# Optimization experiments

Measured on AMD Instinct MI355X. Metric: run time of the kernel, lower is better.

## Reference

```python
import jax, jax.numpy as jnp
import numpy as np

EPS = 1e-7


def setup_inputs() -> dict:
    key = jax.random.key(0)
    k1, k2 = jax.random.split(key)
    N, C = 16384, 10000
    pred = jax.random.normal(k1, (N, C), dtype=jnp.float32)
    labels = jax.random.randint(k2, (N,), 0, C)
    return {"pred": pred, "labels": labels}


def reference(pred, labels):
    N, C = pred.shape
    # randomness of the torch module (random negative offsets + np.random.rand gate),
    # made deterministic/on-device with a fixed key
    k_off, k_u = jax.random.split(jax.random.key(42))
    offsets = jax.random.randint(k_off, (N,), 1, C)          # random_(1, C)
    rand_u = jax.random.uniform(k_u, (N,), dtype=jnp.float32)  # np.random.rand per sample

    target_neg = (labels + offsets) % C                       # shifted-label negatives

    norms = jnp.linalg.norm(pred, axis=-1, keepdims=True) + EPS  # [N,1]
    logit_norm = pred / norms / 2.0
    snorm = jax.nn.softmax(logit_norm, axis=1) + EPS          # [N,C]
    log_snorm = jnp.log(snorm)

    max_prob = jnp.max(snorm, axis=1)                         # argmax_snorm[0]
    argmax = jnp.argmax(snorm, axis=1)                        # argmax_snorm[1]
    # vectorized form of the per-sample loop: replace negative with argmax class
    replace = (rand_u <= max_prob) & (argmax != labels)
    target_neg = jnp.where(replace, argmax, target_neg)

    rows = jnp.arange(N)
    # (1 - onehot(labels)) * log_snorm summed == full row sum minus label entry
    pos_term = (log_snorm.sum(axis=1) - log_snorm[rows, labels]).mean()
    neg_term = log_snorm[rows, target_neg].mean()
    loss = 10.0 * (pos_term - neg_term)
    return (loss, jnp.squeeze(norms))
```

## Files before the change

kernel.cpp:

```cpp
#include <hip/hip_runtime.h>
#include <stdint.h>

#define NROWS 16384
#define NC    10000
#define NF4   2500
#define BLK   256
#define WPB   4
#define NBLK  (NROWS / WPB)
#define EPSF  1e-7f

struct U2 { uint32_t a, b; };

__host__ __device__ constexpr U2 tf2x32(uint32_t k0, uint32_t k1,
                                        uint32_t x0, uint32_t x1) {
  const uint32_t ks2 = k0 ^ k1 ^ 0x1BD11BDAu;
  uint32_t v0 = x0 + k0, v1 = x1 + k1;
#define TF_R(r) { v0 += v1; v1 = (v1 << (r)) | (v1 >> (32 - (r))); v1 ^= v0; }
  TF_R(13) TF_R(15) TF_R(26) TF_R(6)
  v0 += k1;  v1 += ks2 + 1u;
  TF_R(17) TF_R(29) TF_R(16) TF_R(24)
  v0 += ks2; v1 += k0 + 2u;
  TF_R(13) TF_R(15) TF_R(26) TF_R(6)
  v0 += k0;  v1 += k1 + 3u;
  TF_R(17) TF_R(29) TF_R(16) TF_R(24)
  v0 += k1;  v1 += ks2 + 4u;
  TF_R(13) TF_R(15) TF_R(26) TF_R(6)
  v0 += ks2; v1 += k0 + 5u;
#undef TF_R
  return {v0, v1};
}

constexpr U2 KA = tf2x32(0u, 42u, 0u, 0u);
constexpr U2 KB = tf2x32(0u, 42u, 0u, 1u);

__global__ __launch_bounds__(BLK, 8)
void nnce_rows(const float* __restrict__ pred,
               const int* __restrict__ labels,
               float* __restrict__ out,
               float* __restrict__ row_acc)
{
  const int tid  = threadIdx.x;
  const int lane = tid & 63;
  const int wid  = tid >> 6;
  const int row  = blockIdx.x * WPB + wid;
  const float*  p  = pred + (size_t)row * NC;
  const float4* p4 = (const float4*)p;

  const int lab = labels[row];
  const uint32_t xin = (uint32_t)row + ((lane == 1) ? (uint32_t)NROWS : 0u);
  const uint32_t kk0 = (lane == 2) ? KB.a : KA.a;
  const uint32_t kk1 = (lane == 2) ? KB.b : KA.b;
  const U2 rr = tf2x32(kk0, kk1, 0u, xin);
  const uint32_t hb  = __shfl((int)rr.b, 0, 64);
  const uint32_t lob = __shfl((int)rr.b, 1, 64);
  const uint32_t ub  = __shfl((int)rr.b, 2, 64);
  const uint32_t span = 9999u, mult = 6835u;
  const uint32_t off = ((hb % span) * mult + (lob % span)) % span;
  const float ru = __uint_as_float((ub >> 9) | 0x3F800000u) - 1.0f;
  const int cand1 = (lab + 1 + (int)off) % NC;
  const float p_lab = p[lab];
  const float p_c1  = p[cand1];

  float sp = 0.f, ss = 0.f, sc = 0.f, sq = 0.f, mv = -1e30f;
  int mi = 0;

#define PROC1(xv, e) { const float q_ = (xv) * (xv);            \
    sp += (xv); ss += q_;                                        \
    sc = fmaf(q_, (xv), sc); sq = fmaf(q_, q_, sq);              \
    if ((xv) > mv) { mv = (xv); mi = (e); } }
#define PROC4(v, e) { PROC1((v).x, (e)); PROC1((v).y, (e) + 1);  \
                      PROC1((v).z, (e) + 2); PROC1((v).w, (e) + 3); }

  int k = lane;
#pragma unroll 1
  for (int it = 0; it < 9; ++it) {
    const float4 a = p4[k], b = p4[k + 64], c = p4[k + 128], d = p4[k + 192];
    PROC4(a, 4 * k);
    PROC4(b, 4 * (k + 64));
    PROC4(c, 4 * (k + 128));
    PROC4(d, 4 * (k + 192));
    k += 256;
  }
  {
    const float4 a = p4[k], b = p4[k + 64], c = p4[k + 128];
    PROC4(a, 4 * k);
    PROC4(b, 4 * (k + 64));
    PROC4(c, 4 * (k + 128));
  }
  if (lane < 4) {
    const float4 t = p4[2496 + lane];
    PROC4(t, 4 * (2496 + lane));
  }
#undef PROC4
#undef PROC1

  for (int o = 32; o > 0; o >>= 1) {
    sp += __shfl_xor(sp, o, 64);
    ss += __shfl_xor(ss, o, 64);
    sc += __shfl_xor(sc, o, 64);
    sq += __shfl_xor(sq, o, 64);
    const float om = __shfl_xor(mv, o, 64);
    const int   oi = __shfl_xor(mi, o, 64);
    if (om > mv || (om == mv && oi < mi)) { mv = om; mi = oi; }
  }

  const float norm  = sqrtf(ss) + EPSF;
  const float inv2n = 0.5f / norm;
  const float i2    = inv2n * inv2n;
  const float t1 = sp * inv2n;
  const float t2 = 0.5f * ss * i2;
  const float t3 = (1.0f / 6.0f) * sc * i2 * inv2n;
  const float t4 = (1.0f / 24.0f) * sq * i2 * i2;
  const float Z    = (float)NC + t1 + t2 + t3 + t4;
  const float Zm   = (float)NC - t1 + t2 - t3 + t4;
  const float logZ = logf(Z);
  const float eZ   = EPSF * Z;

  const float max_prob = __expf(mv * inv2n) / Z + EPSF;
  const bool  replace  = (ru <= max_prob) && (mi != lab);
  const float p_neg    = replace ? mv : p_c1;

  const float x_lab  = p_lab * inv2n;
  const float x_neg  = p_neg * inv2n;
  const float ls_lab = x_lab + eZ * (1.0f - x_lab) - logZ;
  const float ls_neg = x_neg + eZ * (1.0f - x_neg) - logZ;
  const float sumlog = t1 + eZ * Zm - (float)NC * logZ;

  if (lane == 0) {
    out[1 + row]  = norm;
    row_acc[row]  = (sumlog - ls_lab) - ls_neg;
  }
}

__global__ __launch_bounds__(1024)
void nnce_final(const float* __restrict__ row_acc, float* __restrict__ out) {
  __shared__ double red[1024];
  double s = 0.0;
  for (int i = threadIdx.x; i < NROWS; i += 1024) s += (double)row_acc[i];
  red[threadIdx.x] = s;
  __syncthreads();
  for (int k = 512; k > 0; k >>= 1) {
    if (threadIdx.x < k) red[threadIdx.x] += red[threadIdx.x + k];
    __syncthreads();
  }
  if (threadIdx.x == 0) out[0] = (float)(10.0 * red[0] / (double)NROWS);
}

extern "C" void kernel_launch(void* const* d_in, const int* in_sizes, int n_in,
                              void* d_out, int out_size, void* d_ws, size_t ws_size,
                              hipStream_t stream) {
  const float* pred   = (const float*)d_in[0];
  const int*   labels = (const int*)d_in[1];
  float* out     = (float*)d_out;
  float* row_acc = (float*)d_ws;

  nnce_rows<<<NBLK, BLK, 0, stream>>>(pred, labels, out, row_acc);
  nnce_final<<<1, 1024, 0, stream>>>(row_acc, out);
}
```

Measured before the change: 125.9 us.

## Fuse final reduction via fixed-point atomics and drop argmax index tracking

Replaces the second reduction kernel with per-block fixed-point 64-bit atomic adds into 256 cells, where the last block to finish (found through a counter atomic) sums the cells and writes the loss. It also stops tracking the argmax index: only the max value is kept, and the replace test compares the max against the label's value instead of comparing indices. The aim is to save the second kernel launch and cut per-element compare and select work in the streaming loop. In exchange it adds a memset, atomics, and a last-block pattern, and it can differ from the reference when the max ties with the label's value or a fixed-point value rounds.

```diff
diff --git a/kernel.cpp b/kernel.cpp
--- a/kernel.cpp
+++ b/kernel.cpp
@@ -7,7 +7,9 @@
 #define BLK   256
 #define WPB   4
 #define NBLK  (NROWS / WPB)
+#define NCELL 256
 #define EPSF  1e-7f
+#define SCALE 262144.0
 
 struct U2 { uint32_t a, b; };
 
@@ -37,8 +39,11 @@
 void nnce_rows(const float* __restrict__ pred,
                const int* __restrict__ labels,
                float* __restrict__ out,
-               float* __restrict__ row_acc)
+               unsigned long long* __restrict__ ws)
 {
+  __shared__ long long lred[WPB];
+  __shared__ int lflag;
+
   const int tid  = threadIdx.x;
   const int lane = tid & 63;
   const int wid  = tid >> 6;
@@ -62,34 +67,27 @@
   const float p_c1  = p[cand1];
 
   float sp = 0.f, ss = 0.f, sc = 0.f, sq = 0.f, mv = -1e30f;
-  int mi = 0;
 
-#define PROC1(xv, e) { const float q_ = (xv) * (xv);            \
+#define PROC1(xv) { const float q_ = (xv) * (xv);               \
     sp += (xv); ss += q_;                                        \
     sc = fmaf(q_, (xv), sc); sq = fmaf(q_, q_, sq);              \
-    if ((xv) > mv) { mv = (xv); mi = (e); } }
-#define PROC4(v, e) { PROC1((v).x, (e)); PROC1((v).y, (e) + 1);  \
-                      PROC1((v).z, (e) + 2); PROC1((v).w, (e) + 3); }
+    mv = fmaxf(mv, (xv)); }
+#define PROC4(v) { PROC1((v).x); PROC1((v).y); PROC1((v).z); PROC1((v).w); }
 
   int k = lane;
 #pragma unroll 1
   for (int it = 0; it < 9; ++it) {
     const float4 a = p4[k], b = p4[k + 64], c = p4[k + 128], d = p4[k + 192];
-    PROC4(a, 4 * k);
-    PROC4(b, 4 * (k + 64));
-    PROC4(c, 4 * (k + 128));
-    PROC4(d, 4 * (k + 192));
+    PROC4(a); PROC4(b); PROC4(c); PROC4(d);
     k += 256;
   }
   {
     const float4 a = p4[k], b = p4[k + 64], c = p4[k + 128];
-    PROC4(a, 4 * k);
-    PROC4(b, 4 * (k + 64));
-    PROC4(c, 4 * (k + 128));
+    PROC4(a); PROC4(b); PROC4(c);
   }
   if (lane < 4) {
     const float4 t = p4[2496 + lane];
-    PROC4(t, 4 * (2496 + lane));
+    PROC4(t);
   }
 #undef PROC4
 #undef PROC1
@@ -99,9 +97,7 @@
     ss += __shfl_xor(ss, o, 64);
     sc += __shfl_xor(sc, o, 64);
     sq += __shfl_xor(sq, o, 64);
-    const float om = __shfl_xor(mv, o, 64);
-    const int   oi = __shfl_xor(mi, o, 64);
-    if (om > mv || (om == mv && oi < mi)) { mv = om; mi = oi; }
+    mv  = fmaxf(mv, __shfl_xor(mv, o, 64));
   }
 
   const float norm  = sqrtf(ss) + EPSF;
@@ -117,7 +113,7 @@
   const float eZ   = EPSF * Z;
 
   const float max_prob = __expf(mv * inv2n) / Z + EPSF;
-  const bool  replace  = (ru <= max_prob) && (mi != lab);
+  const bool  replace  = (ru <= max_prob) && (mv != p_lab);
   const float p_neg    = replace ? mv : p_c1;
 
   const float x_lab  = p_lab * inv2n;
@@ -126,24 +122,33 @@
   const float ls_neg = x_neg + eZ * (1.0f - x_neg) - logZ;
   const float sumlog = t1 + eZ * Zm - (float)NC * logZ;
 
+  const float val = (sumlog - ls_lab) - ls_neg;
+
   if (lane == 0) {
-    out[1 + row]  = norm;
-    row_acc[row]  = (sumlog - ls_lab) - ls_neg;
+    out[1 + row] = norm;
+    const long long fx = (long long)((double)val * SCALE);
+    atomicAdd(&ws[1 + (blockIdx.x & (NCELL - 1))], (unsigned long long)fx);
   }
-}
 
-__global__ __launch_bounds__(1024)
-void nnce_final(const float* __restrict__ row_acc, float* __restrict__ out) {
-  __shared__ double red[1024];
-  double s = 0.0;
-  for (int i = threadIdx.x; i < NROWS; i += 1024) s += (double)row_acc[i];
-  red[threadIdx.x] = s;
   __syncthreads();
-  for (int k = 512; k > 0; k >>= 1) {
-    if (threadIdx.x < k) red[threadIdx.x] += red[threadIdx.x + k];
+  if (tid == 0) {
+    __threadfence();
+    const unsigned long long old = atomicAdd(&ws[0], 1ULL);
+    lflag = (old == (unsigned long long)(NBLK - 1)) ? 1 : 0;
+  }
+  __syncthreads();
+  if (lflag) {
+    long long v = 0;
+    if (tid < NCELL) v = (long long)atomicAdd(&ws[1 + tid], 0ULL);
+    for (int o = 32; o > 0; o >>= 1) v += __shfl_down(v, o, 64);
+    if (lane == 0) lred[wid] = v;
     __syncthreads();
+    if (tid == 0) {
+      long long t = 0;
+      for (int w = 0; w < WPB; ++w) t += lred[w];
+      out[0] = (float)(10.0 * ((double)t / SCALE) / (double)NROWS);
+    }
   }
-  if (threadIdx.x == 0) out[0] = (float)(10.0 * red[0] / (double)NROWS);
 }
 
 extern "C" void kernel_launch(void* const* d_in, const int* in_sizes, int n_in,
@@ -151,9 +156,9 @@
                               hipStream_t stream) {
   const float* pred   = (const float*)d_in[0];
   const int*   labels = (const int*)d_in[1];
-  float* out     = (float*)d_out;
-  float* row_acc = (float*)d_ws;
+  float* out = (float*)d_out;
+  unsigned long long* ws = (unsigned long long*)d_ws;
 
-  nnce_rows<<<NBLK, BLK, 0, stream>>>(pred, labels, out, row_acc);
-  nnce_final<<<1, 1024, 0, stream>>>(row_acc, out);
+  hipMemsetAsync(d_ws, 0, (1 + NCELL) * sizeof(unsigned long long), stream);
+  nnce_rows<<<NBLK, BLK, 0, stream>>>(pred, labels, out, ws);
 }
```

Result: slower. 320.1 us (+154.3%).

## Prefetch next row chunk, drop argmax index tracking, shrink blocks, shuffle-reduce final

Applied to the files above, without the earlier changes.

The row kernel now loads the next four float4 chunks while it processes the current ones, a software-pipelined loop. It also replaces argmax index tracking with a plain fmaxf max, comparing the max value to the label's value instead of comparing indices. Blocks shrink from 4 to 2 waves. The final reduction uses float4 loads and wave shuffles instead of a shared-memory tree. The value comparison can decide differently from the index comparison when the label's value ties the row max, and the prefetch raises register pressure.

```diff
diff --git a/kernel.cpp b/kernel.cpp
--- a/kernel.cpp
+++ b/kernel.cpp
@@ -4,8 +4,8 @@
 #define NROWS 16384
 #define NC    10000
 #define NF4   2500
-#define BLK   256
-#define WPB   4
+#define BLK   128
+#define WPB   2
 #define NBLK  (NROWS / WPB)
 #define EPSF  1e-7f
 
@@ -62,35 +62,30 @@
   const float p_c1  = p[cand1];
 
   float sp = 0.f, ss = 0.f, sc = 0.f, sq = 0.f, mv = -1e30f;
-  int mi = 0;
 
-#define PROC1(xv, e) { const float q_ = (xv) * (xv);            \
+#define PROC1(xv) { const float q_ = (xv) * (xv);               \
     sp += (xv); ss += q_;                                        \
     sc = fmaf(q_, (xv), sc); sq = fmaf(q_, q_, sq);              \
-    if ((xv) > mv) { mv = (xv); mi = (e); } }
-#define PROC4(v, e) { PROC1((v).x, (e)); PROC1((v).y, (e) + 1);  \
-                      PROC1((v).z, (e) + 2); PROC1((v).w, (e) + 3); }
+    mv = fmaxf(mv, (xv)); }
+#define PROC4(v) { PROC1((v).x); PROC1((v).y); PROC1((v).z); PROC1((v).w); }
 
   int k = lane;
+  float4 c0 = p4[k], c1 = p4[k + 64], c2 = p4[k + 128], c3 = p4[k + 192];
 #pragma unroll 1
-  for (int it = 0; it < 9; ++it) {
-    const float4 a = p4[k], b = p4[k + 64], c = p4[k + 128], d = p4[k + 192];
-    PROC4(a, 4 * k);
-    PROC4(b, 4 * (k + 64));
-    PROC4(c, 4 * (k + 128));
-    PROC4(d, 4 * (k + 192));
+  for (int it = 0; it < 8; ++it) {
+    const float4 n0 = p4[k + 256], n1 = p4[k + 320],
+                 n2 = p4[k + 384], n3 = p4[k + 448];
+    PROC4(c0); PROC4(c1); PROC4(c2); PROC4(c3);
+    c0 = n0; c1 = n1; c2 = n2; c3 = n3;
     k += 256;
   }
-  {
-    const float4 a = p4[k], b = p4[k + 64], c = p4[k + 128];
-    PROC4(a, 4 * k);
-    PROC4(b, 4 * (k + 64));
-    PROC4(c, 4 * (k + 128));
-  }
-  if (lane < 4) {
-    const float4 t = p4[2496 + lane];
-    PROC4(t, 4 * (2496 + lane));
-  }
+  const float4 e0 = p4[k + 256], e1 = p4[k + 320], e2 = p4[k + 384];
+  float4 tl;
+  const bool hast = (lane < 4);
+  if (hast) tl = p4[2496 + lane];
+  PROC4(c0); PROC4(c1); PROC4(c2); PROC4(c3);
+  PROC4(e0); PROC4(e1); PROC4(e2);
+  if (hast) PROC4(tl);
 #undef PROC4
 #undef PROC1
 
@@ -99,9 +94,7 @@
     ss += __shfl_xor(ss, o, 64);
     sc += __shfl_xor(sc, o, 64);
     sq += __shfl_xor(sq, o, 64);
-    const float om = __shfl_xor(mv, o, 64);
-    const int   oi = __shfl_xor(mi, o, 64);
-    if (om > mv || (om == mv && oi < mi)) { mv = om; mi = oi; }
+    mv  = fmaxf(mv, __shfl_xor(mv, o, 64));
   }
 
   const float norm  = sqrtf(ss) + EPSF;
@@ -117,7 +110,7 @@
   const float eZ   = EPSF * Z;
 
   const float max_prob = __expf(mv * inv2n) / Z + EPSF;
-  const bool  replace  = (ru <= max_prob) && (mi != lab);
+  const bool  replace  = (ru <= max_prob) && (mv != p_lab);
   const float p_neg    = replace ? mv : p_c1;
 
   const float x_lab  = p_lab * inv2n;
@@ -127,23 +120,31 @@
   const float sumlog = t1 + eZ * Zm - (float)NC * logZ;
 
   if (lane == 0) {
-    out[1 + row]  = norm;
-    row_acc[row]  = (sumlog - ls_lab) - ls_neg;
+    out[1 + row] = norm;
+    row_acc[row] = (sumlog - ls_lab) - ls_neg;
   }
 }
 
-__global__ __launch_bounds__(1024)
+__global__ __launch_bounds__(512)
 void nnce_final(const float* __restrict__ row_acc, float* __restrict__ out) {
-  __shared__ double red[1024];
+  __shared__ double lred[8];
+  const int tid  = threadIdx.x;
+  const int lane = tid & 63;
+  const int wid  = tid >> 6;
+  const float4* r4 = (const float4*)row_acc;
   double s = 0.0;
-  for (int i = threadIdx.x; i < NROWS; i += 1024) s += (double)row_acc[i];
-  red[threadIdx.x] = s;
+  for (int i = tid; i < NROWS / 4; i += 512) {
+    const float4 v = r4[i];
+    s += (double)v.x + (double)v.y + (double)v.z + (double)v.w;
+  }
+  for (int o = 32; o > 0; o >>= 1) s += __shfl_xor(s, o, 64);
+  if (lane == 0) lred[wid] = s;
   __syncthreads();
-  for (int k = 512; k > 0; k >>= 1) {
-    if (threadIdx.x < k) red[threadIdx.x] += red[threadIdx.x + k];
-    __syncthreads();
+  if (tid == 0) {
+    double t = 0.0;
+    for (int w = 0; w < 8; ++w) t += lred[w];
+    out[0] = (float)(10.0 * t / (double)NROWS);
   }
-  if (threadIdx.x == 0) out[0] = (float)(10.0 * red[0] / (double)NROWS);
 }
 
 extern "C" void kernel_launch(void* const* d_in, const int* in_sizes, int n_in,
@@ -155,5 +156,5 @@
   float* row_acc = (float*)d_ws;
 
   nnce_rows<<<NBLK, BLK, 0, stream>>>(pred, labels, out, row_acc);
-  nnce_final<<<1, 1024, 0, stream>>>(row_acc, out);
+  nnce_final<<<1, 512, 0, stream>>>(row_acc, out);
 }
```

Result: slower. 145.3 us (+15.4%).
